# Kernel optimization log

Hardware: AMD Instinct MI355X
Metric: run time of the kernel (lower is better)

## Reference

```python
import jax, jax.numpy as jnp
import numpy as np

B, C, H, W, HEADS = 8, 192, 128, 128, 4
EPS = 1e-5  # nn.LayerNorm default eps


def conv_block(x, pw_w, pw_b, dw_w, dw_b):
    # pointwise 1x1 conv (C->C) followed by depthwise 3x3 conv (Restormer-style convBlock)
    x = jnp.einsum('bchw,oc->bohw', x, pw_w) + pw_b[None, :, None, None]
    x = jax.lax.conv_general_dilated(
        x, dw_w, window_strides=(1, 1), padding='SAME',
        dimension_numbers=('NCHW', 'OIHW', 'NCHW'),
        feature_group_count=x.shape[1]) + dw_b[None, :, None, None]
    return x


def setup_inputs() -> dict:
    key = jax.random.key(0)
    ks = jax.random.split(key, 10)
    def n(k, shape, scale=0.02):
        return jax.random.normal(k, shape, jnp.float32) * scale
    return {
        'x': jax.random.normal(ks[0], (B, C, H, W), jnp.float32),
        'ln_w': jnp.ones((C,), jnp.float32),
        'ln_b': jnp.zeros((C,), jnp.float32),
        'q_pw_w': n(ks[1], (C, C)), 'q_pw_b': jnp.zeros((C,), jnp.float32),
        'q_dw_w': n(ks[2], (C, 1, 3, 3)), 'q_dw_b': jnp.zeros((C,), jnp.float32),
        'k_pw_w': n(ks[3], (C, C)), 'k_pw_b': jnp.zeros((C,), jnp.float32),
        'k_dw_w': n(ks[4], (C, 1, 3, 3)), 'k_dw_b': jnp.zeros((C,), jnp.float32),
        'v_pw_w': n(ks[5], (C, C)), 'v_pw_b': jnp.zeros((C,), jnp.float32),
        'v_dw_w': n(ks[6], (C, 1, 3, 3)), 'v_dw_b': jnp.zeros((C,), jnp.float32),
        'f_w': n(ks[7], (C, C)), 'f_b': jnp.zeros((C,), jnp.float32),
        'alpha': jnp.ones((), jnp.float32),
    }


def reference(x, ln_w, ln_b, q_pw_w, q_pw_b, q_dw_w, q_dw_b,
              k_pw_w, k_pw_b, k_dw_w, k_dw_b,
              v_pw_w, v_pw_b, v_dw_w, v_dw_b, f_w, f_b, alpha):
    b, c, h, w = x.shape
    s = c // HEADS
    # LayerNorm over channel axis (x.transpose(1,3) -> LN(last dim=C) -> transpose back)
    xt = jnp.transpose(x, (0, 3, 2, 1))  # (B,W,H,C)
    mu = jnp.mean(xt, axis=-1, keepdims=True)
    var = jnp.var(xt, axis=-1, keepdims=True)
    xt = (xt - mu) * jax.lax.rsqrt(var + EPS) * ln_w + ln_b
    xn = jnp.transpose(xt, (0, 3, 2, 1))  # (B,C,H,W) - normalized; residual uses this

    def flat(t):
        # NCHW -> (B, W*H, C), W-major flatten as in the torch code (transpose(1,3) then reshape)
        return jnp.transpose(t, (0, 3, 2, 1)).reshape(b, w * h, c)

    Q = flat(conv_block(xn, q_pw_w, q_pw_b, q_dw_w, q_dw_b))
    K = flat(conv_block(xn, k_pw_w, k_pw_b, k_dw_w, k_dw_b))
    V = flat(conv_block(xn, v_pw_w, v_pw_b, v_dw_w, v_dw_b))

    def heads(t):
        return jnp.transpose(t.reshape(b, w * h, HEADS, s), (0, 2, 1, 3))  # (B,heads,t,s)

    Qh, Kh, Vh = heads(Q), heads(K), heads(V)
    # channel-wise cross-covariance attention: (s x s) per head, learnable temperature alpha
    att = jax.nn.softmax(jnp.einsum('bhts,bhtq->bhsq', Kh, Qh) / alpha, axis=-1)
    out = jnp.einsum('bhts,bhsq->bhtq', Vh, att)  # (B,heads,t,s)
    # view(b,heads,t,s).transpose(2,3).reshape(b, C, H, W) exactly as in torch
    out = jnp.transpose(out, (0, 1, 3, 2)).reshape(b, c, h, w)
    y = jnp.einsum('bchw,oc->bohw', out, f_w) + f_b[None, :, None, None] + xn
    return y
```

## Files before the change

kernel.cpp:

```cpp
#include <hip/hip_runtime.h>
#include <hip/hip_bf16.h>

#define B_    8
#define C_    192
#define H_    128
#define W_    128
#define HW_   16384
#define HEADS 4
#define S_    48
#define EPS_  1e-5f

typedef __hip_bfloat16 bf16;
typedef unsigned short u16;
typedef __attribute__((ext_vector_type(8))) short short8;
typedef __attribute__((ext_vector_type(4))) short short4v;
typedef __attribute__((ext_vector_type(4))) float f32x4;
typedef __attribute__((ext_vector_type(8))) u16 u16x8;
typedef __attribute__((ext_vector_type(4))) u16 u16x4;
typedef __attribute__((ext_vector_type(2))) u16 u16x2;


__device__ inline float ld(const bf16* p)  { return __bfloat162float(*p); }
__device__ inline void  st(float* p, float v) { *p = v; }
__device__ inline void  st(bf16* p, float v)  { *p = __float2bfloat16(v); }
__device__ inline float b2f(u16 u) {
  unsigned v = (unsigned)u << 16;
  return __builtin_bit_cast(float, v);
}
__device__ inline u16 f2b(float f) {
  return __builtin_bit_cast(u16, __float2bfloat16(f));
}

__global__ __launch_bounds__(256) void zero_kernel(float* p, int n) {
  int i = blockIdx.x * 256 + threadIdx.x;
  if (i < n) p[i] = 0.f;
}

__global__ __launch_bounds__(256) void ln_kernel(
    const float* __restrict__ x, const float* __restrict__ lw,
    const float* __restrict__ lb, bf16* __restrict__ xn) {
  __shared__ float4 sS[8][32];
  __shared__ float4 sQ[8][32];
  int tid = threadIdx.x;
  int g = tid >> 5, q = tid & 31;
  int blk = blockIdx.x;
  int b = blk >> 7;
  int pos = (blk & 127) * 128 + q * 4;
  const float* xp = x + (size_t)b * C_ * HW_ + pos;

  float4 v[3][8];
  float s0 = 0.f, s1 = 0.f, s2 = 0.f, s3 = 0.f;
  float q0 = 0.f, q1 = 0.f, q2 = 0.f, q3 = 0.f;
#pragma unroll
  for (int t = 0; t < 3; t++)
#pragma unroll
    for (int ci = 0; ci < 8; ci++) {
      int c = t * 64 + g * 8 + ci;
      float4 f = *(const float4*)&xp[(size_t)c * HW_];
      v[t][ci] = f;
      s0 += f.x; s1 += f.y; s2 += f.z; s3 += f.w;
      q0 += f.x * f.x; q1 += f.y * f.y; q2 += f.z * f.z; q3 += f.w * f.w;
    }
  sS[g][q] = make_float4(s0, s1, s2, s3);
  sQ[g][q] = make_float4(q0, q1, q2, q3);
  __syncthreads();

  float S[4] = {}, Qs[4] = {};
#pragma unroll
  for (int gg = 0; gg < 8; gg++) {
    float4 a = sS[gg][q];
    float4 bq = sQ[gg][q];
    S[0] += a.x;  S[1] += a.y;  S[2] += a.z;  S[3] += a.w;
    Qs[0] += bq.x; Qs[1] += bq.y; Qs[2] += bq.z; Qs[3] += bq.w;
  }
  float mu[4], r[4];
#pragma unroll
  for (int i = 0; i < 4; i++) {
    mu[i] = S[i] * (1.0f / C_);
    r[i] = rsqrtf(Qs[i] * (1.0f / C_) - mu[i] * mu[i] + EPS_);
  }

  u16* base = (u16*)xn + (size_t)b * C_ * HW_ +
              (size_t)((blk & 127) * 8 + (q >> 2)) * 3072;
#pragma unroll
  for (int t = 0; t < 3; t++) {
#pragma unroll
    for (int j = 0; j < 4; j++) {
      u16x8 o8;
#pragma unroll
      for (int ci = 0; ci < 8; ci++) {
        int c = t * 64 + g * 8 + ci;
        float xv = (j == 0) ? v[t][ci].x : (j == 1) ? v[t][ci].y
                 : (j == 2) ? v[t][ci].z : v[t][ci].w;
        o8[ci] = f2b((xv - mu[j]) * r[j] * lw[c] + lb[c]);
      }
      *(u16x8*)&base[(t * 8 + g) * 128 + ((q & 3) * 4 + j) * 8] = o8;
    }
  }
}

#define SWR 200
template <bool RES, typename OutT>
__global__ __launch_bounds__(256) void pw_mfma_kernel(
    const bf16* __restrict__ in, const float* __restrict__ wt,
    const float* __restrict__ bias, const bf16* __restrict__ residual,
    OutT* __restrict__ out) {
  __shared__ __align__(16) u16 sW[64 * SWR];
  int tid = threadIdx.x;
  int posBase = blockIdx.x * 256;
  int oBase = blockIdx.y * 64;
  int b = blockIdx.z;
  int wv = tid >> 6, lane = tid & 63;
  int quad = lane >> 4, l15 = lane & 15;

#pragma unroll
  for (int i = 0; i < 12; i++) {
    int u = (tid + i * 256) * 4;
    int rr = u / 192, cc = u % 192;
    float4 f = *(const float4*)&wt[(size_t)(oBase + rr) * 192 + cc];
    ushort4 hv;
    hv.x = f2b(f.x); hv.y = f2b(f.y); hv.z = f2b(f.z); hv.w = f2b(f.w);
    *(ushort4*)&sW[rr * SWR + cc] = hv;
  }

  const u16* xb = (const u16*)in + (size_t)b * C_ * HW_ +
                  (size_t)((posBase >> 4) + wv * 4) * 3072 + quad * 128 + l15 * 8;

  short8 bf[3][4];
#pragma unroll
  for (int nt = 0; nt < 4; nt++)
    bf[0][nt] = *(const short8*)&xb[nt * 3072];
#pragma unroll
  for (int nt = 0; nt < 4; nt++)
    bf[1][nt] = *(const short8*)&xb[nt * 3072 + 512];

  __syncthreads();

  f32x4 acc[4][4] = {};
#pragma unroll
  for (int kc = 0; kc < 6; kc++) {
    if (kc < 4) {
#pragma unroll
      for (int nt = 0; nt < 4; nt++)
        bf[(kc + 2) % 3][nt] =
            *(const short8*)&xb[nt * 3072 + (kc + 2) * 512];
    }
    short8 afrag[4];
#pragma unroll
    for (int mt = 0; mt < 4; mt++)
      afrag[mt] = *(const short8*)&sW[(mt * 16 + l15) * SWR + kc * 32 + quad * 8];
#pragma unroll
    for (int nt = 0; nt < 4; nt++)
#pragma unroll
      for (int mt = 0; mt < 4; mt++)
        acc[mt][nt] = __builtin_amdgcn_mfma_f32_16x16x32_bf16(
            afrag[mt], bf[kc % 3][nt], acc[mt][nt], 0, 0, 0);
  }

  const u16* rb = nullptr;
  if (RES)
    rb = (const u16*)residual + (size_t)b * C_ * HW_ +
         (size_t)((posBase >> 4) + wv * 4) * 3072 + l15 * 8;
#pragma unroll
  for (int mt = 0; mt < 4; mt++) {
#pragma unroll
    for (int nt = 0; nt < 4; nt++) {
      u16x4 r4 = {};
      if (RES)
        r4 = *(const u16x4*)&rb[nt * 3072 +
                                ((oBase >> 3) + mt * 2 + (quad >> 1)) * 128 +
                                (quad & 1) * 4];
#pragma unroll
      for (int r = 0; r < 4; r++) {
        int o = oBase + mt * 16 + quad * 4 + r;
        int p = posBase + wv * 64 + nt * 16 + l15;
        float val = acc[mt][nt][r] + bias[o];
        if (RES) val += b2f(r4[r]);
        st(out + ((size_t)b * C_ + o) * HW_ + p, val);
      }
    }
  }
}

__global__ __launch_bounds__(256) void dw_kernel(
    const bf16* __restrict__ in, const float* __restrict__ w9,
    const float* __restrict__ bias, bf16* __restrict__ out) {
  __shared__ __align__(16) u16 sT[18 * 128];
  int blk = blockIdx.x;
  int bc = blk >> 3;
  int h0 = (blk & 7) * 16;
  int c = bc % C_;
  const u16* ip = (const u16*)in + (size_t)bc * HW_;
  int tid = threadIdx.x;

  for (int ch = tid; ch < 288; ch += 256) {
    int r = ch >> 4, g = ch & 15;
    int gh = h0 - 1 + r;
    u16x8 val = {};
    if (gh >= 0 && gh < H_) val = *(const u16x8*)&ip[gh * 128 + g * 8];
    *(u16x8*)&sT[r * 128 + g * 8] = val;
  }
  __syncthreads();

  int r_o = tid >> 4, g = tid & 15;
  const float* wp = w9 + c * 9;
  float acc[8];
#pragma unroll
  for (int j = 0; j < 8; j++) acc[j] = bias[c];
#pragma unroll
  for (int k = 0; k < 3; k++) {
    int rr = r_o + k;
    u16x8 mid = *(const u16x8*)&sT[rr * 128 + g * 8];
    float m[8];
#pragma unroll
    for (int j = 0; j < 8; j++) m[j] = b2f(mid[j]);
    float lv = g ? b2f(sT[rr * 128 + g * 8 - 1]) : 0.f;
    float rv = (g < 15) ? b2f(sT[rr * 128 + g * 8 + 8]) : 0.f;
    float wl = wp[k * 3], wc = wp[k * 3 + 1], wr = wp[k * 3 + 2];
#pragma unroll
    for (int j = 0; j < 8; j++) {
      float left  = (j == 0) ? lv : m[j - 1];
      float right = (j == 7) ? rv : m[j + 1];
      acc[j] += wl * left + wc * m[j] + wr * right;
    }
  }
  u16x8 o;
#pragma unroll
  for (int j = 0; j < 8; j++) o[j] = f2b(acc[j]);
  *(u16x8*)((u16*)out + (size_t)bc * HW_ + (h0 + r_o) * 128 + g * 8) = o;
}

__global__ __launch_bounds__(256) void dwt_kernel(
    const bf16* __restrict__ in, const float* __restrict__ w9,
    const float* __restrict__ bias, bf16* __restrict__ out) {
  __shared__ __align__(16) u16 sIn[130 * 32];
  int blk = blockIdx.x;
  int bc = blk >> 3;
  int w0 = (blk & 7) * 16;
  int c = bc % C_;
  const u16* ip = (const u16*)in + (size_t)bc * HW_;
  int tid = threadIdx.x;

  for (int idx = tid; idx < 520; idx += 256) {
    int r = idx >> 2, seg = idx & 3;
    int h = r - 1;
    int w = w0 - 8 + seg * 8;
    u16x8 val = {};
    if (h >= 0 && h < H_ && w >= 0 && w < W_)
      val = *(const u16x8*)&ip[h * W_ + w];
    int colp = (seg * 8) ^ (((r >> 3) & 3) << 4);
    *(u16x8*)&sIn[r * 32 + colp] = val;
  }
  __syncthreads();

  int wl = tid & 15, ho = tid >> 4;
  const float* wp = w9 + c * 9;
  float wk[9];
#pragma unroll
  for (int i = 0; i < 9; i++) wk[i] = wp[i];
  float bs = bias[c];
  float acc[8];
#pragma unroll
  for (int j = 0; j < 8; j++) acc[j] = bs;
#pragma unroll
  for (int k = 0; k < 10; k++) {
    int r = ho * 8 + k;
    int swz = ((r >> 3) & 3) << 4;
    float lv = b2f(sIn[r * 32 + ((wl + 7) ^ swz)]);
    float mv = b2f(sIn[r * 32 + ((wl + 8) ^ swz)]);
    float rv = b2f(sIn[r * 32 + ((wl + 9) ^ swz)]);
#pragma unroll
    for (int kh = 0; kh < 3; kh++) {
      int j = k - kh;
      if (j >= 0 && j < 8)
        acc[j] += wk[kh * 3] * lv + wk[kh * 3 + 1] * mv + wk[kh * 3 + 2] * rv;
    }
  }
  u16x8 o;
#pragma unroll
  for (int j = 0; j < 8; j++) o[j] = f2b(acc[j]);
  *(u16x8*)((u16*)out + (size_t)bc * HW_ + (w0 + wl) * H_ + ho * 8) = o;
}

__global__ __launch_bounds__(256) void gram_mfma_kernel(
    const bf16* __restrict__ Q, const bf16* __restrict__ K,
    float* __restrict__ logits) {
  __shared__ float sP[4][S_ * S_];
  int bh = blockIdx.y;
  int b = bh >> 2, hd = bh & 3;
  int tid = threadIdx.x;
  int wv = tid >> 6, lane = tid & 63;
  int quad = lane >> 4, l15 = lane & 15;
  const u16* Qb = (const u16*)Q + ((size_t)b * C_ + hd * S_) * HW_;
  const u16* Kb = (const u16*)K + ((size_t)b * C_ + hd * S_) * HW_;
  int pbase = blockIdx.x * 1024 + wv * 256 + quad * 8;

  f32x4 acc[3][3] = {};
#pragma unroll
  for (int t = 0; t < 8; t++) {
    int p = pbase + t * 32;
    short8 a[3], bb[3];
#pragma unroll
    for (int mi = 0; mi < 3; mi++)
      a[mi] = *(const short8*)&Kb[(size_t)(mi * 16 + l15) * HW_ + p];
#pragma unroll
    for (int ni = 0; ni < 3; ni++)
      bb[ni] = *(const short8*)&Qb[(size_t)(ni * 16 + l15) * HW_ + p];
#pragma unroll
    for (int mi = 0; mi < 3; mi++)
#pragma unroll
      for (int ni = 0; ni < 3; ni++)
        acc[mi][ni] = __builtin_amdgcn_mfma_f32_16x16x32_bf16(
            a[mi], bb[ni], acc[mi][ni], 0, 0, 0);
  }

#pragma unroll
  for (int mi = 0; mi < 3; mi++)
#pragma unroll
    for (int r = 0; r < 4; r++) {
      int sk = mi * 16 + quad * 4 + r;
#pragma unroll
      for (int ni = 0; ni < 3; ni++)
        sP[wv][sk * S_ + ni * 16 + l15] = acc[mi][ni][r];
    }
  __syncthreads();

  float* lp = logits + (size_t)bh * S_ * S_;
  for (int e = tid; e < S_ * S_; e += 256)
    atomicAdd(&lp[e], sP[0][e] + sP[1][e] + sP[2][e] + sP[3][e]);
}

__global__ __launch_bounds__(256) void softmax_kernel(
    const float* __restrict__ logits, const float* __restrict__ alpha,
    float* __restrict__ att) {
  int row = blockIdx.x * 256 + threadIdx.x;
  if (row >= B_ * HEADS * S_) return;
  float inv_a = 1.0f / alpha[0];
  const float* lp = logits + (size_t)row * S_;
  float v[S_];
  float m = -1e30f;
  for (int i = 0; i < S_; i++) {
    v[i] = lp[i] * inv_a;
    m = fmaxf(m, v[i]);
  }
  float s = 0.f;
  for (int i = 0; i < S_; i++) { v[i] = expf(v[i] - m); s += v[i]; }
  float inv_s = 1.0f / s;
  float* ap = att + (size_t)row * S_;
  for (int i = 0; i < S_; i++) ap[i] = v[i] * inv_s;
}

#define AVP 264
#define ATP 72
__global__ __launch_bounds__(256) void av_mfma_kernel(
    const bf16* __restrict__ V, const float* __restrict__ att,
    bf16* __restrict__ out) {
  __shared__ __align__(16) u16 sV[64 * AVP];
  __shared__ __align__(16) u16 sA[48 * ATP];
  int bh = blockIdx.y;
  int b = bh >> 2, hd = bh & 3;
  int p0 = blockIdx.x * 256;
  int tid = threadIdx.x;
  int wv = tid >> 6, lane = tid & 63;
  int quad = lane >> 4, l15 = lane & 15;
  const u16* Vb = (const u16*)V + ((size_t)b * C_ + hd * S_) * HW_ + p0;
  const float* ap = att + (size_t)bh * S_ * S_;

#pragma unroll
  for (int i = 0; i < 6; i++) {
    int e = tid + i * 256;
    int s = e >> 5, p8 = (e & 31) * 8;
    u16x8 v8 = *(const u16x8*)&Vb[(size_t)s * HW_ + p8];
    *(u16x8*)&sV[s * AVP + p8] = v8;
  }
  {
    unsigned* zp = (unsigned*)&sV[48 * AVP];
    for (int e = tid; e < 16 * AVP / 2; e += 256) zp[e] = 0;
  }
  for (int e = tid; e < S_ * S_; e += 256) {
    int q = e % S_, s = e / S_;
    sA[q * ATP + s] = f2b(ap[e]);
  }
  for (int e = tid; e < S_ * 16; e += 256) {
    int q = e >> 4, s = 48 + (e & 15);
    sA[q * ATP + s] = 0;
  }
  __syncthreads();

  f32x4 acc[3][4] = {};
#pragma unroll
  for (int kc = 0; kc < 2; kc++) {
    short8 afrag[3];
#pragma unroll
    for (int mt = 0; mt < 3; mt++)
      afrag[mt] = *(const short8*)&sA[(mt * 16 + l15) * ATP + kc * 32 + quad * 8];
#pragma unroll
    for (int nt = 0; nt < 4; nt++) {
      int p = wv * 64 + nt * 16 + l15;
      short8 bfrag;
#pragma unroll
      for (int j = 0; j < 8; j++)
        bfrag[j] = (short)sV[(kc * 32 + quad * 8 + j) * AVP + p];
#pragma unroll
      for (int mt = 0; mt < 3; mt++)
        acc[mt][nt] = __builtin_amdgcn_mfma_f32_16x16x32_bf16(
            afrag[mt], bfrag, acc[mt][nt], 0, 0, 0);
    }
  }

  u16* ob = (u16*)out + (size_t)b * C_ * HW_ + (size_t)(p0 >> 4) * 3072;
#pragma unroll
  for (int mt = 0; mt < 3; mt++)
#pragma unroll
    for (int r = 0; r < 4; r++) {
      int ql = mt * 16 + quad * 4 + r;
      int ch = hd * S_ + ql;
      int cb = (ch >> 3) * 128 + (ch & 7);
#pragma unroll
      for (int nt = 0; nt < 4; nt++)
        ob[(size_t)(wv * 4 + nt) * 3072 + cb + l15 * 8] = f2b(acc[mt][nt][r]);
    }
}

extern "C" void kernel_launch(void* const* d_in, const int* in_sizes, int n_in,
                              void* d_out, int out_size, void* d_ws, size_t ws_size,
                              hipStream_t stream) {
  const float* x      = (const float*)d_in[0];
  const float* ln_w   = (const float*)d_in[1];
  const float* ln_b   = (const float*)d_in[2];
  const float* q_pw_w = (const float*)d_in[3];
  const float* q_pw_b = (const float*)d_in[4];
  const float* q_dw_w = (const float*)d_in[5];
  const float* q_dw_b = (const float*)d_in[6];
  const float* k_pw_w = (const float*)d_in[7];
  const float* k_pw_b = (const float*)d_in[8];
  const float* k_dw_w = (const float*)d_in[9];
  const float* k_dw_b = (const float*)d_in[10];
  const float* v_pw_w = (const float*)d_in[11];
  const float* v_pw_b = (const float*)d_in[12];
  const float* v_dw_w = (const float*)d_in[13];
  const float* v_dw_b = (const float*)d_in[14];
  const float* f_w    = (const float*)d_in[15];
  const float* f_b    = (const float*)d_in[16];
  const float* alpha  = (const float*)d_in[17];
  float* out = (float*)d_out;

  size_t N = (size_t)B_ * C_ * HW_;
  bf16* xn   = (bf16*)d_ws;
  bf16* tmp  = xn + N;
  bf16* A    = tmp + N;
  float* logits = (float*)(A + N);
  float* att    = logits + (size_t)B_ * HEADS * S_ * S_;
  bf16* Kb     = (bf16*)d_out;

  int nlog = B_ * HEADS * S_ * S_;
  zero_kernel<<<dim3(nlog / 256), 256, 0, stream>>>(logits, nlog);

  ln_kernel<<<dim3(B_ * HW_ / 128), 256, 0, stream>>>(x, ln_w, ln_b, xn);

  dim3 gG(HW_ / 256, C_ / 64, B_);
  int dwBlocks = B_ * C_ * 8;

  pw_mfma_kernel<false, bf16><<<gG, 256, 0, stream>>>(xn, q_pw_w, q_pw_b, nullptr, tmp);
  dw_kernel<<<dwBlocks, 256, 0, stream>>>(tmp, q_dw_w, q_dw_b, A);
  pw_mfma_kernel<false, bf16><<<gG, 256, 0, stream>>>(xn, k_pw_w, k_pw_b, nullptr, tmp);
  dw_kernel<<<dwBlocks, 256, 0, stream>>>(tmp, k_dw_w, k_dw_b, Kb);
  gram_mfma_kernel<<<dim3(16, B_ * HEADS), 256, 0, stream>>>(A, Kb, logits);
  softmax_kernel<<<dim3(6), 256, 0, stream>>>(logits, alpha, att);
  pw_mfma_kernel<false, bf16><<<gG, 256, 0, stream>>>(xn, v_pw_w, v_pw_b, nullptr, tmp);
  dwt_kernel<<<dwBlocks, 256, 0, stream>>>(tmp, v_dw_w, v_dw_b, A);
  av_mfma_kernel<<<dim3(HW_ / 256, B_ * HEADS), 256, 0, stream>>>(A, att, tmp);
  pw_mfma_kernel<true, float><<<gG, 256, 0, stream>>>(tmp, f_w, f_b, xn, out);
}
```

Measured before the change: 441.9 us.

## Batch Q/K/V pointwise and depthwise convs into single wider launches

Replaces three separate pointwise GEMM launches with one kernel whose grid z-dimension selects Q, K or V weights, and merges the row and transposed depthwise conv kernels into one launch with a y-dimension selecting the branch. Intermediate buffers are now kept separately per branch (more workspace, and Q/K stored in the output buffer). This cuts launch count and serialization and gives each launch a larger grid to fill the GPU. The cost is a larger memory footprint and less L2 reuse between producer/consumer pairs.

```diff
diff --git a/kernel.cpp b/kernel.cpp
--- a/kernel.cpp
+++ b/kernel.cpp
@@ -182,104 +182,183 @@
   }
 }
 
-__global__ __launch_bounds__(256) void dw_kernel(
-    const bf16* __restrict__ in, const float* __restrict__ w9,
-    const float* __restrict__ bias, bf16* __restrict__ out) {
-  __shared__ __align__(16) u16 sT[18 * 128];
+__global__ __launch_bounds__(256) void pw3_mfma_kernel(
+    const bf16* __restrict__ in,
+    const float* __restrict__ w0, const float* __restrict__ bv0,
+    const float* __restrict__ w1, const float* __restrict__ bv1,
+    const float* __restrict__ w2, const float* __restrict__ bv2,
+    bf16* __restrict__ o0, bf16* __restrict__ o1, bf16* __restrict__ o2) {
+  __shared__ __align__(16) u16 sW[64 * SWR];
+  int tid = threadIdx.x;
+  int posBase = blockIdx.x * 256;
+  int oBase = blockIdx.y * 64;
+  int z = blockIdx.z;
+  int m = z >> 3, b = z & 7;
+  const float* wt   = (m == 0) ? w0  : (m == 1) ? w1  : w2;
+  const float* bias = (m == 0) ? bv0 : (m == 1) ? bv1 : bv2;
+  bf16* out         = (m == 0) ? o0  : (m == 1) ? o1  : o2;
+  int wv = tid >> 6, lane = tid & 63;
+  int quad = lane >> 4, l15 = lane & 15;
+
+#pragma unroll
+  for (int i = 0; i < 12; i++) {
+    int u = (tid + i * 256) * 4;
+    int rr = u / 192, cc = u % 192;
+    float4 f = *(const float4*)&wt[(size_t)(oBase + rr) * 192 + cc];
+    ushort4 hv;
+    hv.x = f2b(f.x); hv.y = f2b(f.y); hv.z = f2b(f.z); hv.w = f2b(f.w);
+    *(ushort4*)&sW[rr * SWR + cc] = hv;
+  }
+
+  const u16* xb = (const u16*)in + (size_t)b * C_ * HW_ +
+                  (size_t)((posBase >> 4) + wv * 4) * 3072 + quad * 128 + l15 * 8;
+
+  short8 bf[3][4];
+#pragma unroll
+  for (int nt = 0; nt < 4; nt++)
+    bf[0][nt] = *(const short8*)&xb[nt * 3072];
+#pragma unroll
+  for (int nt = 0; nt < 4; nt++)
+    bf[1][nt] = *(const short8*)&xb[nt * 3072 + 512];
+
+  __syncthreads();
+
+  f32x4 acc[4][4] = {};
+#pragma unroll
+  for (int kc = 0; kc < 6; kc++) {
+    if (kc < 4) {
+#pragma unroll
+      for (int nt = 0; nt < 4; nt++)
+        bf[(kc + 2) % 3][nt] =
+            *(const short8*)&xb[nt * 3072 + (kc + 2) * 512];
+    }
+    short8 afrag[4];
+#pragma unroll
+    for (int mt = 0; mt < 4; mt++)
+      afrag[mt] = *(const short8*)&sW[(mt * 16 + l15) * SWR + kc * 32 + quad * 8];
+#pragma unroll
+    for (int nt = 0; nt < 4; nt++)
+#pragma unroll
+      for (int mt = 0; mt < 4; mt++)
+        acc[mt][nt] = __builtin_amdgcn_mfma_f32_16x16x32_bf16(
+            afrag[mt], bf[kc % 3][nt], acc[mt][nt], 0, 0, 0);
+  }
+
+#pragma unroll
+  for (int mt = 0; mt < 4; mt++) {
+#pragma unroll
+    for (int nt = 0; nt < 4; nt++) {
+#pragma unroll
+      for (int r = 0; r < 4; r++) {
+        int o = oBase + mt * 16 + quad * 4 + r;
+        int p = posBase + wv * 64 + nt * 16 + l15;
+        st(out + ((size_t)b * C_ + o) * HW_ + p, acc[mt][nt][r] + bias[o]);
+      }
+    }
+  }
+}
+
+__global__ __launch_bounds__(256) void dwc_kernel(
+    const bf16* __restrict__ pQ, const float* __restrict__ wQ,
+    const float* __restrict__ bQ, bf16* __restrict__ oQ,
+    const bf16* __restrict__ pK, const float* __restrict__ wK,
+    const float* __restrict__ bK, bf16* __restrict__ oK,
+    const bf16* __restrict__ pV, const float* __restrict__ wV,
+    const float* __restrict__ bV, bf16* __restrict__ oV) {
+  __shared__ __align__(16) u16 sBuf[130 * 32];
+  int m = blockIdx.y;
   int blk = blockIdx.x;
   int bc = blk >> 3;
-  int h0 = (blk & 7) * 16;
   int c = bc % C_;
-  const u16* ip = (const u16*)in + (size_t)bc * HW_;
   int tid = threadIdx.x;
 
-  for (int ch = tid; ch < 288; ch += 256) {
-    int r = ch >> 4, g = ch & 15;
-    int gh = h0 - 1 + r;
-    u16x8 val = {};
-    if (gh >= 0 && gh < H_) val = *(const u16x8*)&ip[gh * 128 + g * 8];
-    *(u16x8*)&sT[r * 128 + g * 8] = val;
-  }
-  __syncthreads();
-
-  int r_o = tid >> 4, g = tid & 15;
-  const float* wp = w9 + c * 9;
-  float acc[8];
-#pragma unroll
-  for (int j = 0; j < 8; j++) acc[j] = bias[c];
-#pragma unroll
-  for (int k = 0; k < 3; k++) {
-    int rr = r_o + k;
-    u16x8 mid = *(const u16x8*)&sT[rr * 128 + g * 8];
-    float m[8];
-#pragma unroll
-    for (int j = 0; j < 8; j++) m[j] = b2f(mid[j]);
-    float lv = g ? b2f(sT[rr * 128 + g * 8 - 1]) : 0.f;
-    float rv = (g < 15) ? b2f(sT[rr * 128 + g * 8 + 8]) : 0.f;
-    float wl = wp[k * 3], wc = wp[k * 3 + 1], wr = wp[k * 3 + 2];
-#pragma unroll
-    for (int j = 0; j < 8; j++) {
-      float left  = (j == 0) ? lv : m[j - 1];
-      float right = (j == 7) ? rv : m[j + 1];
-      acc[j] += wl * left + wc * m[j] + wr * right;
-    }
-  }
-  u16x8 o;
-#pragma unroll
-  for (int j = 0; j < 8; j++) o[j] = f2b(acc[j]);
-  *(u16x8*)((u16*)out + (size_t)bc * HW_ + (h0 + r_o) * 128 + g * 8) = o;
-}
-
-__global__ __launch_bounds__(256) void dwt_kernel(
-    const bf16* __restrict__ in, const float* __restrict__ w9,
-    const float* __restrict__ bias, bf16* __restrict__ out) {
-  __shared__ __align__(16) u16 sIn[130 * 32];
-  int blk = blockIdx.x;
-  int bc = blk >> 3;
-  int w0 = (blk & 7) * 16;
-  int c = bc % C_;
-  const u16* ip = (const u16*)in + (size_t)bc * HW_;
-  int tid = threadIdx.x;
-
-  for (int idx = tid; idx < 520; idx += 256) {
-    int r = idx >> 2, seg = idx & 3;
-    int h = r - 1;
-    int w = w0 - 8 + seg * 8;
-    u16x8 val = {};
-    if (h >= 0 && h < H_ && w >= 0 && w < W_)
-      val = *(const u16x8*)&ip[h * W_ + w];
-    int colp = (seg * 8) ^ (((r >> 3) & 3) << 4);
-    *(u16x8*)&sIn[r * 32 + colp] = val;
-  }
-  __syncthreads();
-
-  int wl = tid & 15, ho = tid >> 4;
-  const float* wp = w9 + c * 9;
-  float wk[9];
-#pragma unroll
-  for (int i = 0; i < 9; i++) wk[i] = wp[i];
-  float bs = bias[c];
-  float acc[8];
-#pragma unroll
-  for (int j = 0; j < 8; j++) acc[j] = bs;
-#pragma unroll
-  for (int k = 0; k < 10; k++) {
-    int r = ho * 8 + k;
-    int swz = ((r >> 3) & 3) << 4;
-    float lv = b2f(sIn[r * 32 + ((wl + 7) ^ swz)]);
-    float mv = b2f(sIn[r * 32 + ((wl + 8) ^ swz)]);
-    float rv = b2f(sIn[r * 32 + ((wl + 9) ^ swz)]);
-#pragma unroll
-    for (int kh = 0; kh < 3; kh++) {
-      int j = k - kh;
-      if (j >= 0 && j < 8)
-        acc[j] += wk[kh * 3] * lv + wk[kh * 3 + 1] * mv + wk[kh * 3 + 2] * rv;
-    }
-  }
-  u16x8 o;
-#pragma unroll
-  for (int j = 0; j < 8; j++) o[j] = f2b(acc[j]);
-  *(u16x8*)((u16*)out + (size_t)bc * HW_ + (w0 + wl) * H_ + ho * 8) = o;
+  if (m < 2) {
+    const bf16* in = m ? pK : pQ;
+    const float* w9 = m ? wK : wQ;
+    const float* bias = m ? bK : bQ;
+    bf16* out = m ? oK : oQ;
+    int h0 = (blk & 7) * 16;
+    const u16* ip = (const u16*)in + (size_t)bc * HW_;
+
+    for (int ch = tid; ch < 288; ch += 256) {
+      int r = ch >> 4, g = ch & 15;
+      int gh = h0 - 1 + r;
+      u16x8 val = {};
+      if (gh >= 0 && gh < H_) val = *(const u16x8*)&ip[gh * 128 + g * 8];
+      *(u16x8*)&sBuf[r * 128 + g * 8] = val;
+    }
+    __syncthreads();
+
+    int r_o = tid >> 4, g = tid & 15;
+    const float* wp = w9 + c * 9;
+    float acc[8];
+#pragma unroll
+    for (int j = 0; j < 8; j++) acc[j] = bias[c];
+#pragma unroll
+    for (int k = 0; k < 3; k++) {
+      int rr = r_o + k;
+      u16x8 mid = *(const u16x8*)&sBuf[rr * 128 + g * 8];
+      float mv[8];
+#pragma unroll
+      for (int j = 0; j < 8; j++) mv[j] = b2f(mid[j]);
+      float lv = g ? b2f(sBuf[rr * 128 + g * 8 - 1]) : 0.f;
+      float rv = (g < 15) ? b2f(sBuf[rr * 128 + g * 8 + 8]) : 0.f;
+      float wl = wp[k * 3], wc = wp[k * 3 + 1], wr = wp[k * 3 + 2];
+#pragma unroll
+      for (int j = 0; j < 8; j++) {
+        float left  = (j == 0) ? lv : mv[j - 1];
+        float right = (j == 7) ? rv : mv[j + 1];
+        acc[j] += wl * left + wc * mv[j] + wr * right;
+      }
+    }
+    u16x8 o;
+#pragma unroll
+    for (int j = 0; j < 8; j++) o[j] = f2b(acc[j]);
+    *(u16x8*)((u16*)out + (size_t)bc * HW_ + (h0 + r_o) * 128 + g * 8) = o;
+  } else {
+    int w0 = (blk & 7) * 16;
+    const u16* ip = (const u16*)pV + (size_t)bc * HW_;
+
+    for (int idx = tid; idx < 520; idx += 256) {
+      int r = idx >> 2, seg = idx & 3;
+      int h = r - 1;
+      int w = w0 - 8 + seg * 8;
+      u16x8 val = {};
+      if (h >= 0 && h < H_ && w >= 0 && w < W_)
+        val = *(const u16x8*)&ip[h * W_ + w];
+      int colp = (seg * 8) ^ (((r >> 3) & 3) << 4);
+      *(u16x8*)&sBuf[r * 32 + colp] = val;
+    }
+    __syncthreads();
+
+    int wl = tid & 15, ho = tid >> 4;
+    const float* wp = wV + c * 9;
+    float wk[9];
+#pragma unroll
+    for (int i = 0; i < 9; i++) wk[i] = wp[i];
+    float bs = bV[c];
+    float acc[8];
+#pragma unroll
+    for (int j = 0; j < 8; j++) acc[j] = bs;
+#pragma unroll
+    for (int k = 0; k < 10; k++) {
+      int r = ho * 8 + k;
+      int swz = ((r >> 3) & 3) << 4;
+      float lv = b2f(sBuf[r * 32 + ((wl + 7) ^ swz)]);
+      float mv = b2f(sBuf[r * 32 + ((wl + 8) ^ swz)]);
+      float rv = b2f(sBuf[r * 32 + ((wl + 9) ^ swz)]);
+#pragma unroll
+      for (int kh = 0; kh < 3; kh++) {
+        int j = k - kh;
+        if (j >= 0 && j < 8)
+          acc[j] += wk[kh * 3] * lv + wk[kh * 3 + 1] * mv + wk[kh * 3 + 2] * rv;
+      }
+    }
+    u16x8 o;
+#pragma unroll
+    for (int j = 0; j < 8; j++) o[j] = f2b(acc[j]);
+    *(u16x8*)((u16*)oV + (size_t)bc * HW_ + (w0 + wl) * H_ + ho * 8) = o;
+  }
 }
 
 __global__ __launch_bounds__(256) void gram_mfma_kernel(
@@ -447,28 +526,29 @@
 
   size_t N = (size_t)B_ * C_ * HW_;
   bf16* xn   = (bf16*)d_ws;
-  bf16* tmp  = xn + N;
-  bf16* A    = tmp + N;
-  float* logits = (float*)(A + N);
+  bf16* P0   = xn + N;
+  bf16* P1   = P0 + N;
+  bf16* P2   = P1 + N;
+  bf16* Vd   = P2 + N;
+  float* logits = (float*)(Vd + N);
   float* att    = logits + (size_t)B_ * HEADS * S_ * S_;
-  bf16* Kb     = (bf16*)d_out;
+  bf16* Qd = (bf16*)d_out;
+  bf16* Kd = Qd + N;
 
   int nlog = B_ * HEADS * S_ * S_;
   zero_kernel<<<dim3(nlog / 256), 256, 0, stream>>>(logits, nlog);
 
   ln_kernel<<<dim3(B_ * HW_ / 128), 256, 0, stream>>>(x, ln_w, ln_b, xn);
 
-  dim3 gG(HW_ / 256, C_ / 64, B_);
-  int dwBlocks = B_ * C_ * 8;
-
-  pw_mfma_kernel<false, bf16><<<gG, 256, 0, stream>>>(xn, q_pw_w, q_pw_b, nullptr, tmp);
-  dw_kernel<<<dwBlocks, 256, 0, stream>>>(tmp, q_dw_w, q_dw_b, A);
-  pw_mfma_kernel<false, bf16><<<gG, 256, 0, stream>>>(xn, k_pw_w, k_pw_b, nullptr, tmp);
-  dw_kernel<<<dwBlocks, 256, 0, stream>>>(tmp, k_dw_w, k_dw_b, Kb);
-  gram_mfma_kernel<<<dim3(16, B_ * HEADS), 256, 0, stream>>>(A, Kb, logits);
+  pw3_mfma_kernel<<<dim3(HW_ / 256, C_ / 64, 24), 256, 0, stream>>>(
+      xn, q_pw_w, q_pw_b, k_pw_w, k_pw_b, v_pw_w, v_pw_b, P0, P1, P2);
+
+  dwc_kernel<<<dim3(B_ * C_ * 8, 3), 256, 0, stream>>>(
+      P0, q_dw_w, q_dw_b, Qd, P1, k_dw_w, k_dw_b, Kd, P2, v_dw_w, v_dw_b, Vd);
+
+  gram_mfma_kernel<<<dim3(16, B_ * HEADS), 256, 0, stream>>>(Qd, Kd, logits);
   softmax_kernel<<<dim3(6), 256, 0, stream>>>(logits, alpha, att);
-  pw_mfma_kernel<false, bf16><<<gG, 256, 0, stream>>>(xn, v_pw_w, v_pw_b, nullptr, tmp);
-  dwt_kernel<<<dwBlocks, 256, 0, stream>>>(tmp, v_dw_w, v_dw_b, A);
-  av_mfma_kernel<<<dim3(HW_ / 256, B_ * HEADS), 256, 0, stream>>>(A, att, tmp);
-  pw_mfma_kernel<true, float><<<gG, 256, 0, stream>>>(tmp, f_w, f_b, xn, out);
-}
+  av_mfma_kernel<<<dim3(HW_ / 256, B_ * HEADS), 256, 0, stream>>>(Vd, att, P0);
+  pw_mfma_kernel<true, float><<<dim3(HW_ / 256, C_ / 64, B_), 256, 0, stream>>>(
+      P0, f_w, f_b, xn, out);
+}
```

After: 453.7 us. 1.03x slower.
